# Kernel tuning notes

Hardware: AMD Instinct MI355X
Metric: run time of the kernel (lower is better)

The kernel has to match this reference:

```python
import jax, jax.numpy as jnp
import numpy as np

B, S, D = 4, 1024, 4096
HQ, HKV, HD = 32, 8, 128
GROUPS = HQ // HKV
SCALE = 1.0 / np.sqrt(HD)


def setup_inputs() -> dict:
    key = jax.random.key(0)
    ks = jax.random.split(key, 7)
    inv_freq = 1.0 / (10000.0 ** (jnp.arange(0, HD, 2, dtype=jnp.float32) / HD))
    pos = jnp.arange(S, dtype=jnp.float32)
    freqs = pos[:, None] * inv_freq[None, :]           # [S, HD/2]
    emb = jnp.concatenate([freqs, freqs], axis=-1)      # [S, HD] (duplicated halves)
    return {
        "hidden_states": jax.random.normal(ks[0], (B, S, D), dtype=jnp.float32) * 0.02,
        "cos": jnp.cos(emb)[None],                       # [1, S, HD]
        "sin": jnp.sin(emb)[None],                       # [1, S, HD]
        "Wq": jax.random.normal(ks[1], (HQ * HD, D), dtype=jnp.float32) * 0.02,
        "Wk": jax.random.normal(ks[2], (HKV * HD, D), dtype=jnp.float32) * 0.02,
        "Wv": jax.random.normal(ks[3], (HKV * HD, D), dtype=jnp.float32) * 0.02,
        "Wo": jax.random.normal(ks[4], (D, HQ * HD), dtype=jnp.float32) * 0.02,
    }


def _rope(x, cos_h, sin_h):
    # x: [B, S, H, HD]; cos_h/sin_h: [S, HD/2] (non-interleaved rotate-half)
    half = x.shape[-1] // 2
    x1, x2 = x[..., :half], x[..., half:]
    c = cos_h[None, :, None, :]
    s = sin_h[None, :, None, :]
    return jnp.concatenate([x1 * c - x2 * s, x2 * c + x1 * s], axis=-1)


def reference(hidden_states, cos, sin, Wq, Wk, Wv, Wo):
    b, s, d = hidden_states.shape
    # projections (torch Linear: y = x @ W.T)
    q = (hidden_states @ Wq.T).reshape(b, s, HQ, HD)
    k = (hidden_states @ Wk.T).reshape(b, s, HKV, HD)
    v = (hidden_states @ Wv.T).reshape(b, s, HKV, HD)
    # module slices the second half of the [1, S, HD] tables
    cos_h = cos[0, :, HD // 2:]
    sin_h = sin[0, :, HD // 2:]
    q = _rope(q, cos_h, sin_h)
    k = _rope(k, cos_h, sin_h)
    # GQA: repeat each kv head GROUPS times (consecutively, as repeat_kv does)
    k = jnp.repeat(k, GROUPS, axis=2)                    # [B, S, HQ, HD]
    v = jnp.repeat(v, GROUPS, axis=2)
    # full (non-causal) SDPA, as in the source (no mask passed)
    scores = jnp.einsum("bqhd,bkhd->bhqk", q, k) * SCALE
    probs = jax.nn.softmax(scores, axis=-1)
    attn = jnp.einsum("bhqk,bkhd->bqhd", probs, v)
    attn = attn.reshape(b, s, HQ * HD)
    return attn @ Wo.T
```

## Files before the change

### kernel.cpp

```cpp
#include <hip/hip_runtime.h>
#include <hip/hip_bf16.h>
#include <stdint.h>


typedef __attribute__((ext_vector_type(8))) short s8_t;
typedef __attribute__((ext_vector_type(4))) float f4_t;

#define MFMA16(a, b, c) __builtin_amdgcn_mfma_f32_16x16x32_bf16((a), (b), (c), 0, 0, 0)

__device__ __forceinline__ float b2f(unsigned short u) {
  union { unsigned int i; float f; } x; x.i = ((unsigned int)u) << 16; return x.f;
}
__device__ __forceinline__ unsigned short f2b(float f) {
  union { float f; unsigned int i; } x; x.f = f;
  unsigned int r = x.i + 0x7fff + ((x.i >> 16) & 1);
  return (unsigned short)(r >> 16);
}

__device__ __forceinline__ bool probe_is_f32(const void* p) {
  if (!p) return false;
  const unsigned short* u = (const unsigned short*)p;
  bool f = false;
#pragma unroll
  for (int i = 0; i < 64; ++i) {
    const float v = b2f(u[i]);
    f |= !(fabsf(v) < 1e8f);
  }
  return f;
}

__device__ __forceinline__ s8_t load8(const void* base, size_t off, bool f32) {
  if (f32) {
    const float* p = (const float*)base + off;
    const float4 a = *(const float4*)(p);
    const float4 b = *(const float4*)(p + 4);
    union { s8_t v; __hip_bfloat162 h[4]; } t;
    t.h[0] = __float22bfloat162_rn(make_float2(a.x, a.y));
    t.h[1] = __float22bfloat162_rn(make_float2(a.z, a.w));
    t.h[2] = __float22bfloat162_rn(make_float2(b.x, b.y));
    t.h[3] = __float22bfloat162_rn(make_float2(b.z, b.w));
    return t.v;
  }
  return *(const s8_t*)((const unsigned short*)base + off);
}

__global__ __launch_bounds__(256) void gemm_bt(
    void* __restrict__ C,
    const void* __restrict__ A,
    const void* __restrict__ B,
    int M, int N, int K,
    const void* probeA, const void* probeB, const void* probeC)
{
  constexpr int LP = 72;
  __shared__ unsigned short sA[128 * LP];
  __shared__ unsigned short sB[128 * LP];
  const bool fA = probe_is_f32(probeA);
  const bool fB = probe_is_f32(probeB);
  const bool fC = probe_is_f32(probeC);

  const int tid  = threadIdx.x;
  const int lane = tid & 63;
  const int wv   = tid >> 6;
  const int wr   = (wv >> 1) * 64;
  const int wc   = (wv & 1) * 64;
  const int quad = lane >> 4;
  const int l16  = lane & 15;
  const int m0 = blockIdx.x * 128;
  const int n0 = blockIdx.y * 128;

  f4_t acc[4][4];
#pragma unroll
  for (int i = 0; i < 4; ++i)
#pragma unroll
    for (int j = 0; j < 4; ++j) acc[i][j] = (f4_t){0.f, 0.f, 0.f, 0.f};

  int srow[4], scol[4];
#pragma unroll
  for (int it = 0; it < 4; ++it) {
    const int s = it * 256 + tid;
    srow[it] = s >> 3;
    scol[it] = (s & 7) * 8;
  }

  const int nK = K >> 6;
  for (int kt = 0; kt < nK; ++kt) {
    const int k0 = kt << 6;
    s8_t va[4], vb[4];
#pragma unroll
    for (int it = 0; it < 4; ++it) {
      va[it] = load8(A, (size_t)(m0 + srow[it]) * K + k0 + scol[it], fA);
      vb[it] = load8(B, (size_t)(n0 + srow[it]) * K + k0 + scol[it], fB);
    }
#pragma unroll
    for (int it = 0; it < 4; ++it) {
      *(s8_t*)(&sA[srow[it] * LP + scol[it]]) = va[it];
      *(s8_t*)(&sB[srow[it] * LP + scol[it]]) = vb[it];
    }
    __syncthreads();
#pragma unroll
    for (int kc = 0; kc < 2; ++kc) {
      s8_t af[4], bf[4];
#pragma unroll
      for (int i = 0; i < 4; ++i) {
        af[i] = *(const s8_t*)(&sA[(wr + i * 16 + l16) * LP + (kc * 4 + quad) * 8]);
        bf[i] = *(const s8_t*)(&sB[(wc + i * 16 + l16) * LP + (kc * 4 + quad) * 8]);
      }
#pragma unroll
      for (int i = 0; i < 4; ++i)
#pragma unroll
        for (int j = 0; j < 4; ++j)
          acc[i][j] = MFMA16(af[i], bf[j], acc[i][j]);
    }
    __syncthreads();
  }

#pragma unroll
  for (int i = 0; i < 4; ++i) {
    const int rbase = m0 + wr + i * 16 + quad * 4;
#pragma unroll
    for (int j = 0; j < 4; ++j) {
      const int col = n0 + wc + j * 16 + l16;
#pragma unroll
      for (int rg = 0; rg < 4; ++rg) {
        const size_t idx = (size_t)(rbase + rg) * N + col;
        if (fC) ((float*)C)[idx] = acc[i][j][rg];
        else    ((unsigned short*)C)[idx] = f2b(acc[i][j][rg]);
      }
    }
  }
}

__global__ __launch_bounds__(256) void rope_kernel(
    unsigned short* __restrict__ X,
    const void* __restrict__ cosb,
    const void* __restrict__ sinb,
    int log2nh, const void* probe)
{
  const bool f = probe_is_f32(probe);
  const size_t idx = (size_t)blockIdx.x * 256 + threadIdx.x;
  const int j = (int)(idx & 63);
  const size_t row = idx >> 6;
  const int s = (int)((row >> log2nh) & 1023);
  const int ci = s * 128 + 64 + j;
  const float c  = f ? ((const float*)cosb)[ci] : b2f(((const unsigned short*)cosb)[ci]);
  const float sn = f ? ((const float*)sinb)[ci] : b2f(((const unsigned short*)sinb)[ci]);
  unsigned short* p = X + row * 128;
  const float x1 = b2f(p[j]);
  const float x2 = b2f(p[64 + j]);
  p[j]      = f2b(x1 * c - x2 * sn);
  p[64 + j] = f2b(x2 * c + x1 * sn);
}

__global__ __launch_bounds__(256) void attn_kernel(
    unsigned short* O,
    const unsigned short* Q,
    const unsigned short* __restrict__ Kb,
    const unsigned short* __restrict__ Vb)
{
  constexpr int S = 1024, HQ = 32, HKV = 8, HD = 128;
  constexpr int SCP = 1048;
  constexpr int QP  = 152;
  constexpr int VP  = 88;
  constexpr float SCALE = 0.08838834764831845f;
  __shared__ unsigned short sc[16 * SCP];
  __shared__ unsigned short sq[16 * QP];
  __shared__ unsigned short sv[128 * VP];
  __shared__ float s_linv[16];

  const int bid = blockIdx.x;
  const int qt = bid & 63;
  const int h  = (bid >> 6) & 31;
  const int b  = bid >> 11;
  const int kh = h >> 2;
  const int tid  = threadIdx.x;
  const int lane = tid & 63;
  const int wv   = tid >> 6;
  const int quad = lane >> 4;
  const int l16  = lane & 15;

  const unsigned short* Qg = Q  + ((size_t)(b * S + qt * 16) * HQ + h) * HD;
  const unsigned short* Kg = Kb + ((size_t)b * S * HKV + kh) * HD;
  const unsigned short* Vg = Vb + ((size_t)b * S * HKV + kh) * HD;

  {
    const int r = tid >> 4, c = (tid & 15) * 8;
    *(s8_t*)(&sq[r * QP + c]) = *(const s8_t*)(Qg + (size_t)r * (HQ * HD) + c);
  }
  __syncthreads();

#pragma unroll 1
  for (int kt = 0; kt < 16; ++kt) {
    const int ks = wv * 256 + kt * 16;
    f4_t acc = (f4_t){0.f, 0.f, 0.f, 0.f};
#pragma unroll
    for (int kc = 0; kc < 4; ++kc) {
      const s8_t qa = *(const s8_t*)(&sq[l16 * QP + kc * 32 + quad * 8]);
      const s8_t kf = *(const s8_t*)(Kg + (size_t)(ks + l16) * (HKV * HD) + kc * 32 + quad * 8);
      acc = MFMA16(qa, kf, acc);
    }
#pragma unroll
    for (int rg = 0; rg < 4; ++rg)
      sc[(quad * 4 + rg) * SCP + ks + l16] = f2b(acc[rg] * SCALE);
  }
  __syncthreads();

  {
    const int r = tid >> 4, c0 = tid & 15;
    float mx = -1e30f;
#pragma unroll 4
    for (int u = 0; u < 64; ++u)
      mx = fmaxf(mx, b2f(sc[r * SCP + c0 + u * 16]));
#pragma unroll
    for (int off = 8; off; off >>= 1) mx = fmaxf(mx, __shfl_xor(mx, off, 16));
    float sum = 0.f;
#pragma unroll 4
    for (int u = 0; u < 64; ++u) {
      const int idx = r * SCP + c0 + u * 16;
      const float e = __expf(b2f(sc[idx]) - mx);
      sum += e;
      sc[idx] = f2b(e);
    }
#pragma unroll
    for (int off = 8; off; off >>= 1) sum += __shfl_xor(sum, off, 16);
    if (c0 == 0) s_linv[r] = 1.0f / sum;
  }
  __syncthreads();

  f4_t oacc[2];
  oacc[0] = (f4_t){0.f, 0.f, 0.f, 0.f};
  oacc[1] = (f4_t){0.f, 0.f, 0.f, 0.f};
#pragma unroll 1
  for (int ck = 0; ck < 16; ++ck) {
    if (ck) __syncthreads();
#pragma unroll
    for (int it = 0; it < 4; ++it) {
      const int s  = it * 256 + tid;
      const int kk = s >> 4;
      const int c  = (s & 15) * 8;
      const int sw = (s & 7) << 3;
      const s8_t v = *(const s8_t*)(Vg + (size_t)(ck * 64 + kk) * (HKV * HD) + c);
#pragma unroll
      for (int jj = 0; jj < 8; ++jj)
        sv[(c + jj) * VP + (kk ^ sw)] = ((const unsigned short*)&v)[jj];
    }
    __syncthreads();
#pragma unroll
    for (int kc = 0; kc < 2; ++kc) {
      const s8_t pa = *(const s8_t*)(&sc[l16 * SCP + ck * 64 + kc * 32 + quad * 8]);
#pragma unroll
      for (int dt = 0; dt < 2; ++dt) {
        const int d2 = wv * 32 + dt * 16 + l16;
        const s8_t vf = *(const s8_t*)(
            &sv[d2 * VP + ((kc * 32 + quad * 8) ^ (((d2 >> 3) & 7) << 3))]);
        oacc[dt] = MFMA16(pa, vf, oacc[dt]);
      }
    }
  }

#pragma unroll
  for (int dt = 0; dt < 2; ++dt)
#pragma unroll
    for (int rg = 0; rg < 4; ++rg) {
      const int r = quad * 4 + rg;
      const int d = wv * 32 + dt * 16 + l16;
      O[((size_t)(b * S + qt * 16 + r) * HQ + h) * HD + d] =
          f2b(oacc[dt][rg] * s_linv[r]);
    }
}

extern "C" void kernel_launch(void* const* d_in, const int* in_sizes, int n_in,
                              void* d_out, int out_size, void* d_ws, size_t ws_size,
                              hipStream_t stream)
{
  (void)in_sizes; (void)n_in; (void)out_size; (void)ws_size;
  const void* hs   = d_in[0];
  const void* cosb = d_in[1];
  const void* sinb = d_in[2];
  const void* Wq   = d_in[3];
  const void* Wk   = d_in[4];
  const void* Wv   = d_in[5];
  const void* Wo   = d_in[6];

  unsigned short* Qb = (unsigned short*)d_ws;
  unsigned short* Kb = (unsigned short*)d_out;
  unsigned short* Vb = (unsigned short*)d_out + (size_t)4194304;

  gemm_bt<<<dim3(32,  8), 256, 0, stream>>>(Kb, hs, Wk, 4096, 1024, 4096, hs, hs, nullptr);
  gemm_bt<<<dim3(32,  8), 256, 0, stream>>>(Vb, hs, Wv, 4096, 1024, 4096, hs, hs, nullptr);
  gemm_bt<<<dim3(32, 32), 256, 0, stream>>>(Qb, hs, Wq, 4096, 4096, 4096, hs, hs, nullptr);
  rope_kernel<<<32768, 256, 0, stream>>>(Qb, cosb, sinb, 5, hs);
  rope_kernel<<< 8192, 256, 0, stream>>>(Kb, cosb, sinb, 3, hs);
  attn_kernel<<<4 * 32 * 64, 256, 0, stream>>>(Qb, Qb, Kb, Vb);
  gemm_bt<<<dim3(32, 32), 256, 0, stream>>>(d_out, Qb, Wo, 4096, 4096, 4096,
                                            nullptr, hs, hs);
}
```

Before: 2.005 ms.

## Pre-convert inputs to bf16, transpose V, vectorize rope and softmax

Adds a cvt_to_bf16 pass that converts hidden_states, Wq and Wo from fp32 to bf16 once, so the GEMMs no longer convert on every tile load. The V projection now writes V transposed, which lets the attention kernel read V fragments straight from global memory and drops the LDS transpose and its per-chunk barriers. Rope and softmax are vectorized to 8-element accesses, and some loops get unroll 2. The price is extra conversion launches and workspace, and launch choices now depend on in_sizes and buffer sizes.

```diff
diff --git a/kernel.cpp b/kernel.cpp
--- a/kernel.cpp
+++ b/kernel.cpp
@@ -5,6 +5,7 @@
 
 typedef __attribute__((ext_vector_type(8))) short s8_t;
 typedef __attribute__((ext_vector_type(4))) float f4_t;
+typedef __attribute__((ext_vector_type(4))) unsigned short us4_t;
 
 #define MFMA16(a, b, c) __builtin_amdgcn_mfma_f32_16x16x32_bf16((a), (b), (c), 0, 0, 0)
 
@@ -17,9 +18,9 @@
   return (unsigned short)(r >> 16);
 }
 
-__device__ __forceinline__ bool probe_is_f32(const void* p) {
+__device__ __forceinline__ bool probe_is_f32_off(const void* p, int off) {
   if (!p) return false;
-  const unsigned short* u = (const unsigned short*)p;
+  const unsigned short* u = (const unsigned short*)p + off;
   bool f = false;
 #pragma unroll
   for (int i = 0; i < 64; ++i) {
@@ -28,20 +29,33 @@
   }
   return f;
 }
+__device__ __forceinline__ bool probe_is_f32(const void* p) {
+  return probe_is_f32_off(p, 0);
+}
+
+__device__ __forceinline__ s8_t cvt8(const float* p) {
+  const float4 a = *(const float4*)(p);
+  const float4 b = *(const float4*)(p + 4);
+  union { s8_t v; __hip_bfloat162 h[4]; } t;
+  t.h[0] = __float22bfloat162_rn(make_float2(a.x, a.y));
+  t.h[1] = __float22bfloat162_rn(make_float2(a.z, a.w));
+  t.h[2] = __float22bfloat162_rn(make_float2(b.x, b.y));
+  t.h[3] = __float22bfloat162_rn(make_float2(b.z, b.w));
+  return t.v;
+}
 
 __device__ __forceinline__ s8_t load8(const void* base, size_t off, bool f32) {
-  if (f32) {
-    const float* p = (const float*)base + off;
-    const float4 a = *(const float4*)(p);
-    const float4 b = *(const float4*)(p + 4);
-    union { s8_t v; __hip_bfloat162 h[4]; } t;
-    t.h[0] = __float22bfloat162_rn(make_float2(a.x, a.y));
-    t.h[1] = __float22bfloat162_rn(make_float2(a.z, a.w));
-    t.h[2] = __float22bfloat162_rn(make_float2(b.x, b.y));
-    t.h[3] = __float22bfloat162_rn(make_float2(b.z, b.w));
-    return t.v;
-  }
+  if (f32) return cvt8((const float*)base + off);
   return *(const s8_t*)((const unsigned short*)base + off);
+}
+
+__global__ __launch_bounds__(256) void cvt_to_bf16(
+    unsigned short* __restrict__ out, const void* __restrict__ in)
+{
+  const bool f = probe_is_f32(in);
+  const size_t i = ((size_t)blockIdx.x * 256 + threadIdx.x) * 8;
+  if (f) *(s8_t*)(out + i) = cvt8((const float*)in + i);
+  else   *(s8_t*)(out + i) = *(const s8_t*)((const unsigned short*)in + i);
 }
 
 __global__ __launch_bounds__(256) void gemm_bt(
@@ -49,7 +63,8 @@
     const void* __restrict__ A,
     const void* __restrict__ B,
     int M, int N, int K,
-    const void* probeA, const void* probeB, const void* probeC)
+    const void* probeA, const void* probeB, const void* probeC,
+    int transC)
 {
   constexpr int LP = 72;
   __shared__ unsigned short sA[128 * LP];
@@ -114,17 +129,32 @@
     __syncthreads();
   }
 
-#pragma unroll
-  for (int i = 0; i < 4; ++i) {
-    const int rbase = m0 + wr + i * 16 + quad * 4;
-#pragma unroll
-    for (int j = 0; j < 4; ++j) {
-      const int col = n0 + wc + j * 16 + l16;
-#pragma unroll
-      for (int rg = 0; rg < 4; ++rg) {
-        const size_t idx = (size_t)(rbase + rg) * N + col;
-        if (fC) ((float*)C)[idx] = acc[i][j][rg];
-        else    ((unsigned short*)C)[idx] = f2b(acc[i][j][rg]);
+  if (transC) {
+#pragma unroll
+    for (int i = 0; i < 4; ++i) {
+      const int rbase = m0 + wr + i * 16 + quad * 4;
+#pragma unroll
+      for (int j = 0; j < 4; ++j) {
+        const int col = n0 + wc + j * 16 + l16;
+        us4_t t;
+#pragma unroll
+        for (int rg = 0; rg < 4; ++rg) t[rg] = f2b(acc[i][j][rg]);
+        *(us4_t*)(&((unsigned short*)C)[(size_t)col * M + rbase]) = t;
+      }
+    }
+  } else {
+#pragma unroll
+    for (int i = 0; i < 4; ++i) {
+      const int rbase = m0 + wr + i * 16 + quad * 4;
+#pragma unroll
+      for (int j = 0; j < 4; ++j) {
+        const int col = n0 + wc + j * 16 + l16;
+#pragma unroll
+        for (int rg = 0; rg < 4; ++rg) {
+          const size_t idx = (size_t)(rbase + rg) * N + col;
+          if (fC) ((float*)C)[idx] = acc[i][j][rg];
+          else    ((unsigned short*)C)[idx] = f2b(acc[i][j][rg]);
+        }
       }
     }
   }
@@ -134,37 +164,46 @@
     unsigned short* __restrict__ X,
     const void* __restrict__ cosb,
     const void* __restrict__ sinb,
-    int log2nh, const void* probe)
-{
-  const bool f = probe_is_f32(probe);
+    int log2nh, int mode)
+{
+  bool f;
+  if (mode == 1)      f = true;
+  else if (mode == 2) f = false;
+  else f = probe_is_f32_off(cosb, 2048) | probe_is_f32_off(sinb, 2048);
   const size_t idx = (size_t)blockIdx.x * 256 + threadIdx.x;
-  const int j = (int)(idx & 63);
-  const size_t row = idx >> 6;
+  const int jb = (int)(idx & 7) * 8;
+  const size_t row = idx >> 3;
   const int s = (int)((row >> log2nh) & 1023);
-  const int ci = s * 128 + 64 + j;
-  const float c  = f ? ((const float*)cosb)[ci] : b2f(((const unsigned short*)cosb)[ci]);
-  const float sn = f ? ((const float*)sinb)[ci] : b2f(((const unsigned short*)sinb)[ci]);
   unsigned short* p = X + row * 128;
-  const float x1 = b2f(p[j]);
-  const float x2 = b2f(p[64 + j]);
-  p[j]      = f2b(x1 * c - x2 * sn);
-  p[64 + j] = f2b(x2 * c + x1 * sn);
+  union { s8_t v; unsigned short u[8]; } ua, ub, o1, o2;
+  ua.v = *(const s8_t*)(p + jb);
+  ub.v = *(const s8_t*)(p + 64 + jb);
+#pragma unroll
+  for (int j = 0; j < 8; ++j) {
+    const int ci = s * 128 + 64 + jb + j;
+    const float c  = f ? ((const float*)cosb)[ci] : b2f(((const unsigned short*)cosb)[ci]);
+    const float sn = f ? ((const float*)sinb)[ci] : b2f(((const unsigned short*)sinb)[ci]);
+    const float x1 = b2f(ua.u[j]);
+    const float x2 = b2f(ub.u[j]);
+    o1.u[j] = f2b(x1 * c - x2 * sn);
+    o2.u[j] = f2b(x2 * c + x1 * sn);
+  }
+  *(s8_t*)(p + jb)      = o1.v;
+  *(s8_t*)(p + 64 + jb) = o2.v;
 }
 
 __global__ __launch_bounds__(256) void attn_kernel(
     unsigned short* O,
     const unsigned short* Q,
     const unsigned short* __restrict__ Kb,
-    const unsigned short* __restrict__ Vb)
+    const unsigned short* __restrict__ Vt)
 {
   constexpr int S = 1024, HQ = 32, HKV = 8, HD = 128;
   constexpr int SCP = 1048;
   constexpr int QP  = 152;
-  constexpr int VP  = 88;
   constexpr float SCALE = 0.08838834764831845f;
   __shared__ unsigned short sc[16 * SCP];
   __shared__ unsigned short sq[16 * QP];
-  __shared__ unsigned short sv[128 * VP];
   __shared__ float s_linv[16];
 
   const int bid = blockIdx.x;
@@ -180,7 +219,7 @@
 
   const unsigned short* Qg = Q  + ((size_t)(b * S + qt * 16) * HQ + h) * HD;
   const unsigned short* Kg = Kb + ((size_t)b * S * HKV + kh) * HD;
-  const unsigned short* Vg = Vb + ((size_t)b * S * HKV + kh) * HD;
+  const unsigned short* Vg = Vt + ((size_t)kh * HD) * 4096 + (size_t)b * S;
 
   {
     const int r = tid >> 4, c = (tid & 15) * 8;
@@ -188,7 +227,7 @@
   }
   __syncthreads();
 
-#pragma unroll 1
+#pragma unroll 2
   for (int kt = 0; kt < 16; ++kt) {
     const int ks = wv * 256 + kt * 16;
     f4_t acc = (f4_t){0.f, 0.f, 0.f, 0.f};
@@ -206,19 +245,29 @@
 
   {
     const int r = tid >> 4, c0 = tid & 15;
+    unsigned short* srow = &sc[r * SCP + c0 * 8];
     float mx = -1e30f;
-#pragma unroll 4
-    for (int u = 0; u < 64; ++u)
-      mx = fmaxf(mx, b2f(sc[r * SCP + c0 + u * 16]));
+#pragma unroll
+    for (int u = 0; u < 8; ++u) {
+      union { s8_t v; unsigned short us[8]; } t;
+      t.v = *(const s8_t*)(srow + u * 128);
+#pragma unroll
+      for (int j = 0; j < 8; ++j) mx = fmaxf(mx, b2f(t.us[j]));
+    }
 #pragma unroll
     for (int off = 8; off; off >>= 1) mx = fmaxf(mx, __shfl_xor(mx, off, 16));
     float sum = 0.f;
-#pragma unroll 4
-    for (int u = 0; u < 64; ++u) {
-      const int idx = r * SCP + c0 + u * 16;
-      const float e = __expf(b2f(sc[idx]) - mx);
-      sum += e;
-      sc[idx] = f2b(e);
+#pragma unroll
+    for (int u = 0; u < 8; ++u) {
+      union { s8_t v; unsigned short us[8]; } t;
+      t.v = *(const s8_t*)(srow + u * 128);
+#pragma unroll
+      for (int j = 0; j < 8; ++j) {
+        const float e = __expf(b2f(t.us[j]) - mx);
+        sum += e;
+        t.us[j] = f2b(e);
+      }
+      *(s8_t*)(srow + u * 128) = t.v;
     }
 #pragma unroll
     for (int off = 8; off; off >>= 1) sum += __shfl_xor(sum, off, 16);
@@ -229,31 +278,19 @@
   f4_t oacc[2];
   oacc[0] = (f4_t){0.f, 0.f, 0.f, 0.f};
   oacc[1] = (f4_t){0.f, 0.f, 0.f, 0.f};
-#pragma unroll 1
+  const unsigned short* vb0 = Vg + (size_t)(wv * 32 + l16) * 4096 + quad * 8;
+  const unsigned short* vb1 = vb0 + (size_t)16 * 4096;
+  const unsigned short* prow = &sc[l16 * SCP + quad * 8];
+#pragma unroll 2
   for (int ck = 0; ck < 16; ++ck) {
-    if (ck) __syncthreads();
-#pragma unroll
-    for (int it = 0; it < 4; ++it) {
-      const int s  = it * 256 + tid;
-      const int kk = s >> 4;
-      const int c  = (s & 15) * 8;
-      const int sw = (s & 7) << 3;
-      const s8_t v = *(const s8_t*)(Vg + (size_t)(ck * 64 + kk) * (HKV * HD) + c);
-#pragma unroll
-      for (int jj = 0; jj < 8; ++jj)
-        sv[(c + jj) * VP + (kk ^ sw)] = ((const unsigned short*)&v)[jj];
-    }
-    __syncthreads();
 #pragma unroll
     for (int kc = 0; kc < 2; ++kc) {
-      const s8_t pa = *(const s8_t*)(&sc[l16 * SCP + ck * 64 + kc * 32 + quad * 8]);
-#pragma unroll
-      for (int dt = 0; dt < 2; ++dt) {
-        const int d2 = wv * 32 + dt * 16 + l16;
-        const s8_t vf = *(const s8_t*)(
-            &sv[d2 * VP + ((kc * 32 + quad * 8) ^ (((d2 >> 3) & 7) << 3))]);
-        oacc[dt] = MFMA16(pa, vf, oacc[dt]);
-      }
+      const int ko = ck * 64 + kc * 32;
+      const s8_t pa = *(const s8_t*)(prow + ko);
+      const s8_t v0 = *(const s8_t*)(vb0 + ko);
+      const s8_t v1 = *(const s8_t*)(vb1 + ko);
+      oacc[0] = MFMA16(pa, v0, oacc[0]);
+      oacc[1] = MFMA16(pa, v1, oacc[1]);
     }
   }
 
@@ -272,7 +309,6 @@
                               void* d_out, int out_size, void* d_ws, size_t ws_size,
                               hipStream_t stream)
 {
-  (void)in_sizes; (void)n_in; (void)out_size; (void)ws_size;
   const void* hs   = d_in[0];
   const void* cosb = d_in[1];
   const void* sinb = d_in[2];
@@ -281,16 +317,46 @@
   const void* Wv   = d_in[5];
   const void* Wo   = d_in[6];
 
+  const size_t MB = (size_t)1 << 20;
+  const bool f32in = (n_in >= 1 && in_sizes && in_sizes[0] == (int)(64 * MB));
+  int rmode = 0;
+  if (in_sizes && n_in >= 2) {
+    if (in_sizes[1] == 524288) rmode = 1;
+    else if (in_sizes[1] == 262144) rmode = 2;
+  }
+
   unsigned short* Qb = (unsigned short*)d_ws;
   unsigned short* Kb = (unsigned short*)d_out;
-  unsigned short* Vb = (unsigned short*)d_out + (size_t)4194304;
-
-  gemm_bt<<<dim3(32,  8), 256, 0, stream>>>(Kb, hs, Wk, 4096, 1024, 4096, hs, hs, nullptr);
-  gemm_bt<<<dim3(32,  8), 256, 0, stream>>>(Vb, hs, Wv, 4096, 1024, 4096, hs, hs, nullptr);
-  gemm_bt<<<dim3(32, 32), 256, 0, stream>>>(Qb, hs, Wq, 4096, 4096, 4096, hs, hs, nullptr);
-  rope_kernel<<<32768, 256, 0, stream>>>(Qb, cosb, sinb, 5, hs);
-  rope_kernel<<< 8192, 256, 0, stream>>>(Kb, cosb, sinb, 3, hs);
-  attn_kernel<<<4 * 32 * 64, 256, 0, stream>>>(Qb, Qb, Kb, Vb);
-  gemm_bt<<<dim3(32, 32), 256, 0, stream>>>(d_out, Qb, Wo, 4096, 4096, 4096,
-                                            nullptr, hs, hs);
-}
+  unsigned short* Vt = (unsigned short*)d_out + 4194304;
+
+  const void* hsA = hs;
+  if (f32in && out_size >= (int)(48 * MB)) {
+    unsigned short* hs_b = (unsigned short*)d_out + 8388608;
+    cvt_to_bf16<<<8192, 256, 0, stream>>>(hs_b, hs);
+    hsA = hs_b;
+  }
+  const void* WqB = Wq;
+  if (f32in && ws_size >= 64 * MB) {
+    unsigned short* wq_b = (unsigned short*)d_ws + 16777216;
+    cvt_to_bf16<<<8192, 256, 0, stream>>>(wq_b, Wq);
+    WqB = wq_b;
+  }
+  const void* WoB = Wo;
+  if (f32in && ws_size >= 96 * MB) {
+    unsigned short* wo_b = (unsigned short*)d_ws + 33554432;
+    cvt_to_bf16<<<8192, 256, 0, stream>>>(wo_b, Wo);
+    WoB = wo_b;
+  }
+
+  gemm_bt<<<dim3(32,  8), 256, 0, stream>>>(Kb, hsA, Wk, 4096, 1024, 4096,
+                                            hsA, Wk, nullptr, 0);
+  gemm_bt<<<dim3(32,  8), 256, 0, stream>>>(Vt, hsA, Wv, 4096, 1024, 4096,
+                                            hsA, Wv, nullptr, 1);
+  gemm_bt<<<dim3(32, 32), 256, 0, stream>>>(Qb, hsA, WqB, 4096, 4096, 4096,
+                                            hsA, WqB, nullptr, 0);
+  rope_kernel<<<4096, 256, 0, stream>>>(Qb, cosb, sinb, 5, rmode);
+  rope_kernel<<<1024, 256, 0, stream>>>(Kb, cosb, sinb, 3, rmode);
+  attn_kernel<<<4 * 32 * 64, 256, 0, stream>>>(Qb, Qb, Kb, Vt);
+  gemm_bt<<<dim3(32, 32), 256, 0, stream>>>(d_out, Qb, WoB, 4096, 4096, 4096,
+                                            nullptr, WoB, hs, 0);
+}
```

New measurement: 1.939 ms. 1.03x faster.
